# Optimization experiments

Measured on AMD Instinct MI355X. Metric: run time of the kernel, lower is better.

The kernel has to match this reference:

```python
import math
import jax, jax.numpy as jnp
import numpy as np


def setup_inputs() -> dict:
    key = jax.random.key(0)
    k0, k1, k2 = jax.random.split(key, 3)
    b, c, h, w = 4, 256, 64, 64
    x = jax.random.normal(k0, (b, c, h, w), dtype=jnp.float32)
    # 1x1 conv weights stored as [out_ch, in_ch]
    qkv_w = jax.random.normal(k1, (3 * c, c), dtype=jnp.float32) / math.sqrt(c)
    qkv_b = jnp.zeros((3 * c,), dtype=jnp.float32)
    out_w = jax.random.normal(k2, (c, c), dtype=jnp.float32) / math.sqrt(c)
    out_b = jnp.zeros((c,), dtype=jnp.float32)
    return {"x": x, "qkv_w": qkv_w, "qkv_b": qkv_b, "out_w": out_w, "out_b": out_b}


def reference(x, qkv_w, qkv_b, out_w, out_b):
    b, c, h, w = x.shape
    n = h * w
    # 1x1 conv QKV projection: [b, 3c, h, w]
    qkv = jnp.einsum('oc,bchw->bohw', qkv_w, x) + qkv_b[None, :, None, None]
    # chunk along channels into q, k, v each [b, c, n]
    qkv = qkv.reshape(b, 3, c, n)
    q, k, v = qkv[:, 0], qkv[:, 1], qkv[:, 2]
    # attn[b, i, j] = sum_c k[b,c,i] * q[b,c,j] / sqrt(c); softmax over key axis (dim=-2 -> axis=1)
    scores = jnp.einsum('bcn,bcm->bnm', k, q) / math.sqrt(c)
    attn = jax.nn.softmax(scores, axis=1)
    # out[b, c, j] = sum_i v[b,c,i] * attn[b,i,j]
    o = jnp.einsum('bcn,bnm->bcm', v, attn).reshape(b, c, h, w)
    # output 1x1 conv
    return jnp.einsum('oc,bchw->bohw', out_w, o) + out_b[None, :, None, None]
```

## Files before the change

### kernel.cpp

```cpp
#include <hip/hip_runtime.h>

typedef unsigned short u16;
typedef unsigned int u32;
typedef __attribute__((ext_vector_type(8))) short short8;
typedef __attribute__((ext_vector_type(4))) short short4v;
typedef __attribute__((ext_vector_type(16))) float f32x16;

#define MFMA32 __builtin_amdgcn_mfma_f32_32x32x16_bf16

#define NSEQ 4096
#define CD 256
#define CF 0.09016844005556021f

__device__ __forceinline__ u16 f2bf(float f) {
  u32 u = __float_as_uint(f);
  u += 0x7fffu + ((u >> 16) & 1u);
  return (u16)(u >> 16);
}
__device__ __forceinline__ float bf2f(short s) {
  return __uint_as_float(((u32)(u16)s) << 16);
}
__device__ __forceinline__ void async16(const void* g, void* l) {
  __builtin_amdgcn_global_load_lds(
      (const __attribute__((address_space(1))) u32*)g,
      (__attribute__((address_space(3))) u32*)l, 16, 0, 0);
}

__global__ void cast_w(const float* __restrict__ qkv_w,
                       const float* __restrict__ out_w, u16* __restrict__ wq,
                       u16* __restrict__ wo) {
  int idx = blockIdx.x * 256 + threadIdx.x;
  if (idx < 768 * CD) wq[idx] = f2bf(qkv_w[idx]);
  if (idx < CD * CD) wo[idx] = f2bf(out_w[idx]);
}

__global__ __launch_bounds__(256) void xpose(const float* __restrict__ x,
                                             u16* __restrict__ x_t) {
  __shared__ float tile[64][65];
  const int t = threadIdx.x;
  const int b = blockIdx.z;
  const int n0 = blockIdx.x * 64, c0 = blockIdx.y * 64;
  const float* xb = x + (size_t)b * CD * NSEQ;
  const int cr = t >> 4, nc4 = (t & 15) * 4;
#pragma unroll
  for (int i = 0; i < 4; ++i) {
    int c = cr + 16 * i;
    float4 v = *(const float4*)(xb + (size_t)(c0 + c) * NSEQ + n0 + nc4);
    tile[c][nc4 + 0] = v.x;
    tile[c][nc4 + 1] = v.y;
    tile[c][nc4 + 2] = v.z;
    tile[c][nc4 + 3] = v.w;
  }
  __syncthreads();
  const int n = t & 63, cc = (t >> 6) * 16;
  u16* dst = x_t + (size_t)b * NSEQ * CD + (size_t)(n0 + n) * CD + c0 + cc;
#pragma unroll
  for (int j = 0; j < 4; ++j) {
    short4v pv;
#pragma unroll
    for (int r = 0; r < 4; ++r) pv[r] = (short)f2bf(tile[cc + 4 * j + r][n]);
    *(short4v*)(dst + 4 * j) = pv;
  }
}

__global__ __launch_bounds__(256, 2) void qkv_gemm2(
    const u16* __restrict__ wq, const float* __restrict__ qkv_b,
    const u16* __restrict__ x_t, u16* __restrict__ q_t, u16* __restrict__ k_t,
    u16* __restrict__ v_) {
  __shared__ u16 __align__(16) Wls[64 * 256];
  __shared__ u16 __align__(16) Bls[64 * 256];
  const int t = threadIdx.x, w = t >> 6, lane = t & 63;
  const int l31 = lane & 31, l5 = lane >> 5;
  const int oh = w & 1, nh2 = w >> 1;
  const int n0 = blockIdx.x * 64, o0 = blockIdx.y * 64, b = blockIdx.z;
  const u16* Xb = x_t + (size_t)b * NSEQ * CD;
#pragma unroll
  for (int j = 0; j < 8; ++j) {
    int r = w * 16 + j * 2 + l5;
    async16(wq + (size_t)(o0 + r) * CD + ((l31 ^ (r & 7)) * 8),
            Wls + (w * 16 + j * 2) * 256);
    async16(Xb + (size_t)(n0 + r) * CD + ((l31 ^ (r & 7)) * 8),
            Bls + (w * 16 + j * 2) * 256);
  }
  __builtin_amdgcn_s_waitcnt(0);
  __syncthreads();
  f32x16 acc;
#pragma unroll
  for (int i = 0; i < 16; ++i) acc[i] = 0.f;
  const int ra = oh * 32 + l31, rb = nh2 * 32 + l31;
#pragma unroll
  for (int kc = 0; kc < 16; ++kc) {
    short8 a = *(const short8*)(Wls + ra * 256 + (((kc * 2 + l5) ^ (ra & 7)) * 8));
    short8 bb = *(const short8*)(Bls + rb * 256 + (((kc * 2 + l5) ^ (rb & 7)) * 8));
    acc = MFMA32(a, bb, acc, 0, 0, 0);
  }
  const int n_g = n0 + nh2 * 32 + l31;
  const int otype = blockIdx.y >> 2;
  if (otype < 2) {
    u16* dst = (otype == 0 ? q_t : k_t) + (size_t)b * NSEQ * CD + (size_t)n_g * CD;
    const int cb0 = o0 - otype * 256 + oh * 32;
#pragma unroll
    for (int g = 0; g < 4; ++g) {
      float4 bv = *(const float4*)(qkv_b + o0 + oh * 32 + g * 8 + l5 * 4);
      const float* bp = (const float*)&bv;
      short4v pk;
#pragma unroll
      for (int r = 0; r < 4; ++r) pk[r] = (short)f2bf(acc[g * 4 + r] + bp[r]);
      *(short4v*)(dst + cb0 + g * 8 + l5 * 4) = pk;
    }
  } else {
    u16* dst = v_ + (size_t)b * CD * NSEQ;
#pragma unroll
    for (int g = 0; g < 4; ++g) {
      float4 bv = *(const float4*)(qkv_b + o0 + oh * 32 + g * 8 + l5 * 4);
      const float* bp = (const float*)&bv;
#pragma unroll
      for (int r = 0; r < 4; ++r) {
        int c = o0 - 512 + oh * 32 + g * 8 + l5 * 4 + r;
        dst[(size_t)c * NSEQ + n_g] = f2bf(acc[g * 4 + r] + bp[r]);
      }
    }
  }
}

__global__ __launch_bounds__(512, 2) void flash5(const u16* __restrict__ q_t,
                                                 const u16* __restrict__ k_t,
                                                 const u16* __restrict__ v_,
                                                 u16* __restrict__ opart,
                                                 float2* __restrict__ ml) {
  __shared__ u16 __align__(16) Kls[2][64 * 256];
  __shared__ u16 __align__(16) Vls[2][256 * 64];
  __shared__ u16 __align__(16) Pls[128 * 72];
  __shared__ float pmax[2][128];
  __shared__ float psum[2][128];

  const int t = threadIdx.x, w = t >> 6, lane = t & 63;
  const int l31 = lane & 31, l5 = lane >> 5;
  const int g = w >> 2, nh = w & 1, mh = (w >> 1) & 1;

  const int linear = blockIdx.x;
  const int xcd = linear & 7, slot = linear >> 3;
  const int b = xcd >> 1;
  const int sub = (xcd & 1) * 32 + slot;
  const int mblk = sub & 31, half = sub >> 5;
  const int m0 = mblk * 128;
  const int nbase = half * 2048;

  const u16* Qb = q_t + (size_t)b * NSEQ * CD;
  const u16* Kb = k_t + (size_t)b * NSEQ * CD;
  const u16* Vb = v_ + (size_t)b * CD * NSEQ;

  const int lm = g * 64 + mh * 32 + l31;
  const int mrow = m0 + lm;

  short8 qf[16];
#pragma unroll
  for (int kc = 0; kc < 16; ++kc)
    qf[kc] = *(const short8*)(Qb + (size_t)mrow * CD + kc * 16 + l5 * 8);

  const int kr = w * 8;
  const int vrb = w * 32;
  const int vr_lane = lane >> 3, vc_lane = lane & 7;

#pragma unroll
  for (int j = 0; j < 4; ++j) {
    int r = kr + j * 2 + l5;
    async16(Kb + (size_t)(nbase + r) * CD + ((l31 ^ (r & 7)) * 8),
            &Kls[0][(kr + j * 2) * 256]);
    int rv = vrb + j * 8 + vr_lane;
    async16(Vb + (size_t)rv * NSEQ + nbase + ((vc_lane ^ (rv & 7)) * 8),
            &Vls[0][(vrb + j * 8) * 64]);
  }

  float mst = -3.0e38f, lst = 0.f;
  f32x16 oa[4];
#pragma unroll
  for (int i = 0; i < 4; ++i)
#pragma unroll
    for (int r = 0; r < 16; ++r) oa[i][r] = 0.f;

  for (int tt = 0; tt < 32; ++tt) {
    const int cur = tt & 1;
    __builtin_amdgcn_s_waitcnt(0);
    __syncthreads();
    if (tt + 1 < 32) {
      const int n0 = nbase + (tt + 1) * 64;
      const int nxt = cur ^ 1;
#pragma unroll
      for (int j = 0; j < 4; ++j) {
        int r = kr + j * 2 + l5;
        async16(Kb + (size_t)(n0 + r) * CD + ((l31 ^ (r & 7)) * 8),
                &Kls[nxt][(kr + j * 2) * 256]);
        int rv = vrb + j * 8 + vr_lane;
        async16(Vb + (size_t)rv * NSEQ + n0 + ((vc_lane ^ (rv & 7)) * 8),
                &Vls[nxt][(vrb + j * 8) * 64]);
      }
    }
    f32x16 s;
#pragma unroll
    for (int i = 0; i < 16; ++i) s[i] = 0.f;
    const int rk = nh * 32 + l31;
#pragma unroll
    for (int kc = 0; kc < 16; ++kc) {
      short8 a =
          *(const short8*)(&Kls[cur][rk * 256 + (((kc * 2 + l5) ^ (rk & 7)) * 8)]);
      s = MFMA32(a, qf[kc], s, 0, 0, 0);
    }
    float rm = s[0];
#pragma unroll
    for (int i = 1; i < 16; ++i) rm = fmaxf(rm, s[i]);
    rm = fmaxf(rm, __shfl_xor(rm, 32));
    if (lane < 32) pmax[nh][g * 64 + mh * 32 + lane] = rm;
    __syncthreads();
    float rb = fmaxf(pmax[0][lm], pmax[1][lm]);
    float mnew = fmaxf(mst, rb * CF);
    float al = exp2f(mst - mnew);
    mst = mnew;
    float ls = 0.f;
#pragma unroll
    for (int gg = 0; gg < 4; ++gg) {
      short4v pk;
#pragma unroll
      for (int r = 0; r < 4; ++r) {
        float p = exp2f(s[gg * 4 + r] * CF - mnew);
        ls += p;
        pk[r] = (short)f2bf(p);
      }
      *(short4v*)(Pls + lm * 72 + nh * 32 + gg * 8 + l5 * 4) = pk;
    }
    ls += __shfl_xor(ls, 32);
    if (lane < 32) psum[nh][g * 64 + mh * 32 + lane] = ls;
    __syncthreads();
    lst = lst * al + psum[0][lm] + psum[1][lm];
    if (__ballot(al != 1.0f)) {
#pragma unroll
      for (int i = 0; i < 4; ++i)
#pragma unroll
        for (int r = 0; r < 16; ++r) oa[i][r] *= al;
    }
#pragma unroll
    for (int nb = 0; nb < 4; ++nb) {
      short8 pf = *(const short8*)(Pls + lm * 72 + nb * 16 + l5 * 8);
#pragma unroll
      for (int ct = 0; ct < 4; ++ct) {
        int c = nh * 128 + ct * 32 + l31;
        short8 vf =
            *(const short8*)(&Vls[cur][c * 64 + (((nb * 2 + l5) ^ (c & 7)) * 8)]);
        oa[ct] = MFMA32(vf, pf, oa[ct], 0, 0, 0);
      }
    }
  }

  float inv = 1.0f / lst;
  u16* dst = opart + ((size_t)(half * 4 + b) * NSEQ + mrow) * CD;
#pragma unroll
  for (int ct = 0; ct < 4; ++ct)
#pragma unroll
    for (int gg = 0; gg < 4; ++gg) {
      short4v pk;
#pragma unroll
      for (int r = 0; r < 4; ++r) pk[r] = (short)f2bf(oa[ct][gg * 4 + r] * inv);
      *(short4v*)(dst + nh * 128 + ct * 32 + gg * 8 + l5 * 4) = pk;
    }
  if (nh == 0 && lane < 32)
    ml[(size_t)(half * 4 + b) * NSEQ + m0 + g * 64 + mh * 32 + lane] =
        make_float2(mst, lst);
}

__global__ __launch_bounds__(256, 2) void out_gemm4(
    const u16* __restrict__ wo, const float* __restrict__ out_b,
    const u16* __restrict__ opart, const float2* __restrict__ ml,
    float* __restrict__ out) {
  __shared__ u16 __align__(16) Wls[64 * 256];
  __shared__ u16 __align__(16) Bls[64 * 256];
  const int t = threadIdx.x, w = t >> 6, lane = t & 63;
  const int l31 = lane & 31, l5 = lane >> 5;
  const int oh = w & 1, nh2 = w >> 1;
  const int n0 = blockIdx.x * 64, o0 = blockIdx.y * 64, b = blockIdx.z;
#pragma unroll
  for (int j = 0; j < 8; ++j) {
    int r = w * 16 + j * 2 + l5;
    async16(wo + (size_t)(o0 + r) * CD + ((l31 ^ (r & 7)) * 8),
            Wls + (w * 16 + j * 2) * 256);
  }
  const u16* O1 = opart + (size_t)b * NSEQ * CD;
  const u16* O2 = opart + (size_t)(4 + b) * NSEQ * CD;
  const float2* ml1 = ml + (size_t)b * NSEQ;
  const float2* ml2 = ml + (size_t)(4 + b) * NSEQ;
#pragma unroll
  for (int i = 0; i < 8; ++i) {
    int idx = i * 256 + t;
    int r = idx >> 5, p = idx & 31;
    int n = n0 + r;
    float2 s1 = ml1[n], s2 = ml2[n];
    float M = fmaxf(s1.x, s2.x);
    float w1 = s1.y * exp2f(s1.x - M), w2 = s2.y * exp2f(s2.x - M);
    float inv = 1.0f / (w1 + w2);
    w1 *= inv;
    w2 *= inv;
    short8 x1 = *(const short8*)(O1 + (size_t)n * CD + p * 8);
    short8 x2 = *(const short8*)(O2 + (size_t)n * CD + p * 8);
    short8 om;
#pragma unroll
    for (int e = 0; e < 8; ++e)
      om[e] = (short)f2bf(w1 * bf2f(x1[e]) + w2 * bf2f(x2[e]));
    *(short8*)(Bls + r * 256 + ((p ^ (r & 7)) * 8)) = om;
  }
  __builtin_amdgcn_s_waitcnt(0);
  __syncthreads();
  f32x16 acc;
#pragma unroll
  for (int i = 0; i < 16; ++i) acc[i] = 0.f;
  const int ra = oh * 32 + l31, rb = nh2 * 32 + l31;
#pragma unroll
  for (int kc = 0; kc < 16; ++kc) {
    short8 a = *(const short8*)(Wls + ra * 256 + (((kc * 2 + l5) ^ (ra & 7)) * 8));
    short8 bb = *(const short8*)(Bls + rb * 256 + (((kc * 2 + l5) ^ (rb & 7)) * 8));
    acc = MFMA32(a, bb, acc, 0, 0, 0);
  }
  const int n_g = n0 + nh2 * 32 + l31;
#pragma unroll
  for (int g = 0; g < 4; ++g) {
    float4 bv = *(const float4*)(out_b + o0 + oh * 32 + g * 8 + l5 * 4);
    const float* bp = (const float*)&bv;
#pragma unroll
    for (int r = 0; r < 4; ++r) {
      int o = o0 + oh * 32 + g * 8 + l5 * 4 + r;
      out[((size_t)b * CD + o) * NSEQ + n_g] = acc[g * 4 + r] + bp[r];
    }
  }
}

extern "C" void kernel_launch(void* const* d_in, const int* in_sizes, int n_in,
                              void* d_out, int out_size, void* d_ws,
                              size_t ws_size, hipStream_t stream) {
  const float* x = (const float*)d_in[0];
  const float* qkv_w = (const float*)d_in[1];
  const float* qkv_b = (const float*)d_in[2];
  const float* out_w = (const float*)d_in[3];
  const float* out_b = (const float*)d_in[4];
  float* out = (float*)d_out;

  const size_t SZ = (size_t)4 * NSEQ * CD;
  u16* x_t = (u16*)d_ws;
  u16* q_t = x_t + SZ;
  u16* k_t = q_t + SZ;
  u16* v_ = k_t + SZ;
  u16* opart = v_ + SZ;
  u16* wq = opart + 2 * SZ;
  u16* wo = wq + 768 * CD;
  float2* ml = (float2*)(wo + CD * CD);

  dim3 blk(256);
  cast_w<<<dim3(768), blk, 0, stream>>>(qkv_w, out_w, wq, wo);
  xpose<<<dim3(64, 4, 4), blk, 0, stream>>>(x, x_t);
  qkv_gemm2<<<dim3(64, 12, 4), blk, 0, stream>>>(wq, qkv_b, x_t, q_t, k_t, v_);
  flash5<<<dim3(256), dim3(512), 0, stream>>>(q_t, k_t, v_, opart, ml);
  out_gemm4<<<dim3(64, 4, 4), blk, 0, stream>>>(wo, out_b, opart, ml, out);
}
```

Before: 217.5 us.

## Enlarge GEMM tiles to 128x128 and restructure flash kernel to avoid LDS P staging

Both projection GEMMs move to 512-thread blocks computing 128x128 tiles with two accumulators per wave, halving the grid and increasing operand reuse from LDS. The flash kernel is reorganized so each wave owns 32 query rows across the full 64-key tile. The row max and sum are then computed within the wave, and P is repacked into MFMA operands via lane shuffles instead of being written to shared memory. This removes the pmax/psum/Pls LDS buffers and two block barriers per iteration, at the cost of more registers per wave and occupancy lowered to one block per CU. The block-to-(batch, half, m-block) mapping in the flash kernel is also changed.

```diff
diff --git a/kernel.cpp b/kernel.cpp
--- a/kernel.cpp
+++ b/kernel.cpp
@@ -1,4 +1,5 @@
 #include <hip/hip_runtime.h>
+#include <hip/hip_bf16.h>
 
 typedef unsigned short u16;
 typedef unsigned int u32;
@@ -19,6 +20,14 @@
 }
 __device__ __forceinline__ float bf2f(short s) {
   return __uint_as_float(((u32)(u16)s) << 16);
+}
+__device__ __forceinline__ u32 pk2bf(float a, float b) {
+  union {
+    __hip_bfloat162 h;
+    u32 u;
+  } cv;
+  cv.h = __float22bfloat162_rn(make_float2(a, b));
+  return cv.u;
 }
 __device__ __forceinline__ void async16(const void* g, void* l) {
   __builtin_amdgcn_global_load_lds(
@@ -63,16 +72,16 @@
   }
 }
 
-__global__ __launch_bounds__(256, 2) void qkv_gemm2(
+__global__ __launch_bounds__(512, 1) void qkv_gemm3(
     const u16* __restrict__ wq, const float* __restrict__ qkv_b,
     const u16* __restrict__ x_t, u16* __restrict__ q_t, u16* __restrict__ k_t,
     u16* __restrict__ v_) {
-  __shared__ u16 __align__(16) Wls[64 * 256];
-  __shared__ u16 __align__(16) Bls[64 * 256];
+  __shared__ u16 __align__(16) Wls[128 * 256];
+  __shared__ u16 __align__(16) Bls[128 * 256];
   const int t = threadIdx.x, w = t >> 6, lane = t & 63;
   const int l31 = lane & 31, l5 = lane >> 5;
-  const int oh = w & 1, nh2 = w >> 1;
-  const int n0 = blockIdx.x * 64, o0 = blockIdx.y * 64, b = blockIdx.z;
+  const int os = w & 3, nh = w >> 2;
+  const int n0 = blockIdx.x * 128, o0 = blockIdx.y * 128, b = blockIdx.z;
   const u16* Xb = x_t + (size_t)b * NSEQ * CD;
 #pragma unroll
   for (int j = 0; j < 8; ++j) {
@@ -84,73 +93,79 @@
   }
   __builtin_amdgcn_s_waitcnt(0);
   __syncthreads();
-  f32x16 acc;
-#pragma unroll
-  for (int i = 0; i < 16; ++i) acc[i] = 0.f;
-  const int ra = oh * 32 + l31, rb = nh2 * 32 + l31;
+  f32x16 acc0, acc1;
+#pragma unroll
+  for (int i = 0; i < 16; ++i) {
+    acc0[i] = 0.f;
+    acc1[i] = 0.f;
+  }
+  const int ra = os * 32 + l31;
+  const int rb0 = nh * 64 + l31, rb1 = rb0 + 32;
 #pragma unroll
   for (int kc = 0; kc < 16; ++kc) {
     short8 a = *(const short8*)(Wls + ra * 256 + (((kc * 2 + l5) ^ (ra & 7)) * 8));
-    short8 bb = *(const short8*)(Bls + rb * 256 + (((kc * 2 + l5) ^ (rb & 7)) * 8));
-    acc = MFMA32(a, bb, acc, 0, 0, 0);
-  }
-  const int n_g = n0 + nh2 * 32 + l31;
-  const int otype = blockIdx.y >> 2;
-  if (otype < 2) {
-    u16* dst = (otype == 0 ? q_t : k_t) + (size_t)b * NSEQ * CD + (size_t)n_g * CD;
-    const int cb0 = o0 - otype * 256 + oh * 32;
-#pragma unroll
-    for (int g = 0; g < 4; ++g) {
-      float4 bv = *(const float4*)(qkv_b + o0 + oh * 32 + g * 8 + l5 * 4);
-      const float* bp = (const float*)&bv;
-      short4v pk;
-#pragma unroll
-      for (int r = 0; r < 4; ++r) pk[r] = (short)f2bf(acc[g * 4 + r] + bp[r]);
-      *(short4v*)(dst + cb0 + g * 8 + l5 * 4) = pk;
-    }
-  } else {
-    u16* dst = v_ + (size_t)b * CD * NSEQ;
-#pragma unroll
-    for (int g = 0; g < 4; ++g) {
-      float4 bv = *(const float4*)(qkv_b + o0 + oh * 32 + g * 8 + l5 * 4);
-      const float* bp = (const float*)&bv;
-#pragma unroll
-      for (int r = 0; r < 4; ++r) {
-        int c = o0 - 512 + oh * 32 + g * 8 + l5 * 4 + r;
-        dst[(size_t)c * NSEQ + n_g] = f2bf(acc[g * 4 + r] + bp[r]);
-      }
-    }
-  }
-}
-
-__global__ __launch_bounds__(512, 2) void flash5(const u16* __restrict__ q_t,
+    short8 b0 = *(const short8*)(Bls + rb0 * 256 + (((kc * 2 + l5) ^ (rb0 & 7)) * 8));
+    short8 b1 = *(const short8*)(Bls + rb1 * 256 + (((kc * 2 + l5) ^ (rb1 & 7)) * 8));
+    acc0 = MFMA32(a, b0, acc0, 0, 0, 0);
+    acc1 = MFMA32(a, b1, acc1, 0, 0, 0);
+  }
+  const int otype = blockIdx.y >> 1;
+  const int obase = o0 + os * 32;
+#pragma unroll
+  for (int na = 0; na < 2; ++na) {
+    f32x16& acc = na ? acc1 : acc0;
+    const int n_g = n0 + nh * 64 + na * 32 + l31;
+    if (otype < 2) {
+      u16* dst = (otype == 0 ? q_t : k_t) + (size_t)b * NSEQ * CD +
+                 (size_t)n_g * CD + (obase - otype * 256);
+#pragma unroll
+      for (int g = 0; g < 4; ++g) {
+        float4 bv = *(const float4*)(qkv_b + obase + g * 8 + l5 * 4);
+        const float* bp = (const float*)&bv;
+        short4v pk;
+#pragma unroll
+        for (int r = 0; r < 4; ++r) pk[r] = (short)f2bf(acc[g * 4 + r] + bp[r]);
+        *(short4v*)(dst + g * 8 + l5 * 4) = pk;
+      }
+    } else {
+      u16* dst = v_ + (size_t)b * CD * NSEQ;
+#pragma unroll
+      for (int g = 0; g < 4; ++g) {
+        float4 bv = *(const float4*)(qkv_b + obase + g * 8 + l5 * 4);
+        const float* bp = (const float*)&bv;
+#pragma unroll
+        for (int r = 0; r < 4; ++r) {
+          int c = obase - 512 + g * 8 + l5 * 4 + r;
+          dst[(size_t)c * NSEQ + n_g] = f2bf(acc[g * 4 + r] + bp[r]);
+        }
+      }
+    }
+  }
+}
+
+__global__ __launch_bounds__(512, 1) void flash6(const u16* __restrict__ q_t,
                                                  const u16* __restrict__ k_t,
                                                  const u16* __restrict__ v_,
                                                  u16* __restrict__ opart,
                                                  float2* __restrict__ ml) {
   __shared__ u16 __align__(16) Kls[2][64 * 256];
   __shared__ u16 __align__(16) Vls[2][256 * 64];
-  __shared__ u16 __align__(16) Pls[128 * 72];
-  __shared__ float pmax[2][128];
-  __shared__ float psum[2][128];
 
   const int t = threadIdx.x, w = t >> 6, lane = t & 63;
   const int l31 = lane & 31, l5 = lane >> 5;
-  const int g = w >> 2, nh = w & 1, mh = (w >> 1) & 1;
+  const int s = w >> 1, ch = (w & 1) * 128;
 
   const int linear = blockIdx.x;
   const int xcd = linear & 7, slot = linear >> 3;
-  const int b = xcd >> 1;
-  const int sub = (xcd & 1) * 32 + slot;
-  const int mblk = sub & 31, half = sub >> 5;
-  const int m0 = mblk * 128;
+  const int b = xcd >> 1, half = xcd & 1;
+  const int m0 = slot * 128;
   const int nbase = half * 2048;
 
   const u16* Qb = q_t + (size_t)b * NSEQ * CD;
   const u16* Kb = k_t + (size_t)b * NSEQ * CD;
   const u16* Vb = v_ + (size_t)b * CD * NSEQ;
 
-  const int lm = g * 64 + mh * 32 + l31;
+  const int lm = s * 32 + l31;
   const int mrow = m0 + lm;
 
   short8 qf[16];
@@ -196,87 +211,113 @@
                 &Vls[nxt][(vrb + j * 8) * 64]);
       }
     }
-    f32x16 s;
-#pragma unroll
-    for (int i = 0; i < 16; ++i) s[i] = 0.f;
-    const int rk = nh * 32 + l31;
+    f32x16 sa, sb;
+#pragma unroll
+    for (int i = 0; i < 16; ++i) {
+      sa[i] = 0.f;
+      sb[i] = 0.f;
+    }
+    const int rk0 = l31, rk1 = 32 + l31;
 #pragma unroll
     for (int kc = 0; kc < 16; ++kc) {
-      short8 a =
-          *(const short8*)(&Kls[cur][rk * 256 + (((kc * 2 + l5) ^ (rk & 7)) * 8)]);
-      s = MFMA32(a, qf[kc], s, 0, 0, 0);
-    }
-    float rm = s[0];
-#pragma unroll
-    for (int i = 1; i < 16; ++i) rm = fmaxf(rm, s[i]);
+      short8 a0 =
+          *(const short8*)(&Kls[cur][rk0 * 256 + (((kc * 2 + l5) ^ (l31 & 7)) * 8)]);
+      short8 a1 =
+          *(const short8*)(&Kls[cur][rk1 * 256 + (((kc * 2 + l5) ^ (l31 & 7)) * 8)]);
+      sa = MFMA32(a0, qf[kc], sa, 0, 0, 0);
+      sb = MFMA32(a1, qf[kc], sb, 0, 0, 0);
+    }
+    float rm = sa[0];
+#pragma unroll
+    for (int i = 1; i < 16; ++i) rm = fmaxf(rm, sa[i]);
+#pragma unroll
+    for (int i = 0; i < 16; ++i) rm = fmaxf(rm, sb[i]);
     rm = fmaxf(rm, __shfl_xor(rm, 32));
-    if (lane < 32) pmax[nh][g * 64 + mh * 32 + lane] = rm;
-    __syncthreads();
-    float rb = fmaxf(pmax[0][lm], pmax[1][lm]);
-    float mnew = fmaxf(mst, rb * CF);
+    float mnew = fmaxf(mst, rm * CF);
     float al = exp2f(mst - mnew);
     mst = mnew;
+    u32 d[2][4][2];
     float ls = 0.f;
+#pragma unroll
+    for (int a = 0; a < 2; ++a) {
+      f32x16& sv = a ? sb : sa;
+#pragma unroll
+      for (int gg = 0; gg < 4; ++gg) {
+        float p0 = exp2f(sv[gg * 4 + 0] * CF - mnew);
+        float p1 = exp2f(sv[gg * 4 + 1] * CF - mnew);
+        float p2 = exp2f(sv[gg * 4 + 2] * CF - mnew);
+        float p3 = exp2f(sv[gg * 4 + 3] * CF - mnew);
+        ls += (p0 + p1) + (p2 + p3);
+        d[a][gg][0] = pk2bf(p0, p1);
+        d[a][gg][1] = pk2bf(p2, p3);
+      }
+    }
+    ls += __shfl_xor(ls, 32);
+    lst = lst * al + ls;
+    if (__ballot(al != 1.0f)) {
+#pragma unroll
+      for (int i = 0; i < 4; ++i)
+#pragma unroll
+        for (int r = 0; r < 16; ++r) oa[i][r] *= al;
+    }
+    short8 pf[4];
+#pragma unroll
+    for (int f = 0; f < 4; ++f) {
+      const int a = f >> 1, g0 = (f & 1) * 2;
+      u32 n0d = d[a][g0][0], n1d = d[a][g0][1];
+      u32 m0d = d[a][g0 + 1][0], m1d = d[a][g0 + 1][1];
+      u32 s0 = l5 ? n0d : m0d;
+      u32 s1 = l5 ? n1d : m1d;
+      u32 e0 = (u32)__shfl_xor((int)s0, 32);
+      u32 e1 = (u32)__shfl_xor((int)s1, 32);
+      union {
+        u32 u[4];
+        short8 s8;
+      } cv;
+      cv.u[0] = l5 ? e0 : n0d;
+      cv.u[1] = l5 ? e1 : n1d;
+      cv.u[2] = l5 ? m0d : e0;
+      cv.u[3] = l5 ? m1d : e1;
+      pf[f] = cv.s8;
+    }
+#pragma unroll
+    for (int f = 0; f < 4; ++f) {
+#pragma unroll
+      for (int ct = 0; ct < 4; ++ct) {
+        int c = ch + ct * 32 + l31;
+        short8 vf =
+            *(const short8*)(&Vls[cur][c * 64 + (((f * 2 + l5) ^ (c & 7)) * 8)]);
+        oa[ct] = MFMA32(vf, pf[f], oa[ct], 0, 0, 0);
+      }
+    }
+  }
+
+  float inv = 1.0f / lst;
+  u16* dst = opart + ((size_t)(half * 4 + b) * NSEQ + mrow) * CD;
+#pragma unroll
+  for (int ct = 0; ct < 4; ++ct)
 #pragma unroll
     for (int gg = 0; gg < 4; ++gg) {
       short4v pk;
 #pragma unroll
-      for (int r = 0; r < 4; ++r) {
-        float p = exp2f(s[gg * 4 + r] * CF - mnew);
-        ls += p;
-        pk[r] = (short)f2bf(p);
-      }
-      *(short4v*)(Pls + lm * 72 + nh * 32 + gg * 8 + l5 * 4) = pk;
-    }
-    ls += __shfl_xor(ls, 32);
-    if (lane < 32) psum[nh][g * 64 + mh * 32 + lane] = ls;
-    __syncthreads();
-    lst = lst * al + psum[0][lm] + psum[1][lm];
-    if (__ballot(al != 1.0f)) {
-#pragma unroll
-      for (int i = 0; i < 4; ++i)
-#pragma unroll
-        for (int r = 0; r < 16; ++r) oa[i][r] *= al;
-    }
-#pragma unroll
-    for (int nb = 0; nb < 4; ++nb) {
-      short8 pf = *(const short8*)(Pls + lm * 72 + nb * 16 + l5 * 8);
-#pragma unroll
-      for (int ct = 0; ct < 4; ++ct) {
-        int c = nh * 128 + ct * 32 + l31;
-        short8 vf =
-            *(const short8*)(&Vls[cur][c * 64 + (((nb * 2 + l5) ^ (c & 7)) * 8)]);
-        oa[ct] = MFMA32(vf, pf, oa[ct], 0, 0, 0);
-      }
-    }
-  }
-
-  float inv = 1.0f / lst;
-  u16* dst = opart + ((size_t)(half * 4 + b) * NSEQ + mrow) * CD;
-#pragma unroll
-  for (int ct = 0; ct < 4; ++ct)
-#pragma unroll
-    for (int gg = 0; gg < 4; ++gg) {
-      short4v pk;
-#pragma unroll
       for (int r = 0; r < 4; ++r) pk[r] = (short)f2bf(oa[ct][gg * 4 + r] * inv);
-      *(short4v*)(dst + nh * 128 + ct * 32 + gg * 8 + l5 * 4) = pk;
-    }
-  if (nh == 0 && lane < 32)
-    ml[(size_t)(half * 4 + b) * NSEQ + m0 + g * 64 + mh * 32 + lane] =
+      *(short4v*)(dst + ch + ct * 32 + gg * 8 + l5 * 4) = pk;
+    }
+  if ((w & 1) == 0 && lane < 32)
+    ml[(size_t)(half * 4 + b) * NSEQ + m0 + s * 32 + lane] =
         make_float2(mst, lst);
 }
 
-__global__ __launch_bounds__(256, 2) void out_gemm4(
+__global__ __launch_bounds__(512, 1) void out_gemm5(
     const u16* __restrict__ wo, const float* __restrict__ out_b,
     const u16* __restrict__ opart, const float2* __restrict__ ml,
     float* __restrict__ out) {
-  __shared__ u16 __align__(16) Wls[64 * 256];
-  __shared__ u16 __align__(16) Bls[64 * 256];
+  __shared__ u16 __align__(16) Wls[128 * 256];
+  __shared__ u16 __align__(16) Bls[128 * 256];
   const int t = threadIdx.x, w = t >> 6, lane = t & 63;
   const int l31 = lane & 31, l5 = lane >> 5;
-  const int oh = w & 1, nh2 = w >> 1;
-  const int n0 = blockIdx.x * 64, o0 = blockIdx.y * 64, b = blockIdx.z;
+  const int os = w & 3, nh = w >> 2;
+  const int n0 = blockIdx.x * 128, o0 = blockIdx.y * 128, b = blockIdx.z;
 #pragma unroll
   for (int j = 0; j < 8; ++j) {
     int r = w * 16 + j * 2 + l5;
@@ -289,7 +330,7 @@
   const float2* ml2 = ml + (size_t)(4 + b) * NSEQ;
 #pragma unroll
   for (int i = 0; i < 8; ++i) {
-    int idx = i * 256 + t;
+    int idx = i * 512 + t;
     int r = idx >> 5, p = idx & 31;
     int n = n0 + r;
     float2 s1 = ml1[n], s2 = ml2[n];
@@ -308,25 +349,36 @@
   }
   __builtin_amdgcn_s_waitcnt(0);
   __syncthreads();
-  f32x16 acc;
-#pragma unroll
-  for (int i = 0; i < 16; ++i) acc[i] = 0.f;
-  const int ra = oh * 32 + l31, rb = nh2 * 32 + l31;
+  f32x16 acc0, acc1;
+#pragma unroll
+  for (int i = 0; i < 16; ++i) {
+    acc0[i] = 0.f;
+    acc1[i] = 0.f;
+  }
+  const int ra = os * 32 + l31;
+  const int rb0 = nh * 64 + l31, rb1 = rb0 + 32;
 #pragma unroll
   for (int kc = 0; kc < 16; ++kc) {
     short8 a = *(const short8*)(Wls + ra * 256 + (((kc * 2 + l5) ^ (ra & 7)) * 8));
-    short8 bb = *(const short8*)(Bls + rb * 256 + (((kc * 2 + l5) ^ (rb & 7)) * 8));
-    acc = MFMA32(a, bb, acc, 0, 0, 0);
-  }
-  const int n_g = n0 + nh2 * 32 + l31;
-#pragma unroll
-  for (int g = 0; g < 4; ++g) {
-    float4 bv = *(const float4*)(out_b + o0 + oh * 32 + g * 8 + l5 * 4);
-    const float* bp = (const float*)&bv;
-#pragma unroll
-    for (int r = 0; r < 4; ++r) {
-      int o = o0 + oh * 32 + g * 8 + l5 * 4 + r;
-      out[((size_t)b * CD + o) * NSEQ + n_g] = acc[g * 4 + r] + bp[r];
+    short8 b0 = *(const short8*)(Bls + rb0 * 256 + (((kc * 2 + l5) ^ (rb0 & 7)) * 8));
+    short8 b1 = *(const short8*)(Bls + rb1 * 256 + (((kc * 2 + l5) ^ (rb1 & 7)) * 8));
+    acc0 = MFMA32(a, b0, acc0, 0, 0, 0);
+    acc1 = MFMA32(a, b1, acc1, 0, 0, 0);
+  }
+  const int obase = o0 + os * 32;
+#pragma unroll
+  for (int na = 0; na < 2; ++na) {
+    f32x16& acc = na ? acc1 : acc0;
+    const int n_g = n0 + nh * 64 + na * 32 + l31;
+#pragma unroll
+    for (int g = 0; g < 4; ++g) {
+      float4 bv = *(const float4*)(out_b + obase + g * 8 + l5 * 4);
+      const float* bp = (const float*)&bv;
+#pragma unroll
+      for (int r = 0; r < 4; ++r) {
+        int o = obase + g * 8 + l5 * 4 + r;
+        out[((size_t)b * CD + o) * NSEQ + n_g] = acc[g * 4 + r] + bp[r];
+      }
     }
   }
 }
@@ -351,10 +403,11 @@
   u16* wo = wq + 768 * CD;
   float2* ml = (float2*)(wo + CD * CD);
 
-  dim3 blk(256);
-  cast_w<<<dim3(768), blk, 0, stream>>>(qkv_w, out_w, wq, wo);
-  xpose<<<dim3(64, 4, 4), blk, 0, stream>>>(x, x_t);
-  qkv_gemm2<<<dim3(64, 12, 4), blk, 0, stream>>>(wq, qkv_b, x_t, q_t, k_t, v_);
-  flash5<<<dim3(256), dim3(512), 0, stream>>>(q_t, k_t, v_, opart, ml);
-  out_gemm4<<<dim3(64, 4, 4), blk, 0, stream>>>(wo, out_b, opart, ml, out);
-}
+  cast_w<<<dim3(768), dim3(256), 0, stream>>>(qkv_w, out_w, wq, wo);
+  xpose<<<dim3(64, 4, 4), dim3(256), 0, stream>>>(x, x_t);
+  qkv_gemm3<<<dim3(32, 6, 4), dim3(512), 0, stream>>>(wq, qkv_b, x_t, q_t, k_t,
+                                                      v_);
+  flash6<<<dim3(256), dim3(512), 0, stream>>>(q_t, k_t, v_, opart, ml);
+  out_gemm5<<<dim3(32, 2, 4), dim3(512), 0, stream>>>(wo, out_b, opart, ml,
+                                                      out);
+}
```

After: 231.2 us. 6.3% more time.
